# Optimization experiments

Measured on AMD Instinct MI355X. Metric: run time of the kernel, lower is better.

The kernel has to match this reference:

```python
import jax, jax.numpy as jnp
import numpy as np

B, S, D, H = 2, 2048, 1024, 16
HD = D // H
SCALE = HD ** -0.5

def setup_inputs() -> dict:
    key = jax.random.key(0)
    ks = jax.random.split(key, 5)
    x = jax.random.normal(ks[0], (B, S, D), dtype=jnp.float32)
    Wqkv = jax.random.normal(ks[1], (D, 3 * D), dtype=jnp.float32) * (D ** -0.5)
    bqkv = jnp.zeros((3 * D,), dtype=jnp.float32)
    Wproj = jax.random.normal(ks[2], (D, D), dtype=jnp.float32) * (D ** -0.5)
    bproj = jnp.zeros((D,), dtype=jnp.float32)
    return {"x": x, "Wqkv": Wqkv, "bqkv": bqkv, "Wproj": Wproj, "bproj": bproj}

def reference(x, Wqkv, bqkv, Wproj, bproj):
    b, s, _ = x.shape
    qkv = x @ Wqkv + bqkv                       # [B,S,3D]
    qkv = qkv.reshape(b, s, 3, H, HD)
    q, k, v = [jnp.transpose(qkv[:, :, i], (0, 2, 1, 3)) for i in range(3)]  # [B,H,S,HD]
    attn = jnp.einsum('bhqd,bhkd->bhqk', q, k) * SCALE   # [B,H,S,S]
    attn = jax.nn.softmax(attn, axis=-1)
    out = jnp.einsum('bhqk,bhkd->bhqd', attn, v)         # [B,H,S,HD]
    out = jnp.transpose(out, (0, 2, 1, 3)).reshape(b, s, D)
    return out @ Wproj + bproj
```

## Files before the change

kernel.cpp:

```cpp
#include <hip/hip_runtime.h>
#include <hip/hip_bf16.h>

#define BB 2
#define SS 2048
#define DD 1024
#define HH 16
#define HDD 64
#define MM (BB*SS)
#define NQKV (3*DD)
#define SCALE 0.125f
#define QPRESCALE 0.18033688f

typedef __bf16 bf16_t;
typedef bf16_t bf16x4 __attribute__((ext_vector_type(4)));
typedef bf16_t bf16x8 __attribute__((ext_vector_type(8)));
typedef float f32x4 __attribute__((ext_vector_type(4)));
typedef float f32x16 __attribute__((ext_vector_type(16)));

__device__ __forceinline__ void gl_lds16(const bf16_t* g, bf16_t* l) {
    __builtin_amdgcn_global_load_lds(
        (const __attribute__((address_space(1))) unsigned int*)(uintptr_t)g,
        (__attribute__((address_space(3))) unsigned int*)(uintptr_t)l,
        16, 0, 0);
}

__global__ __launch_bounds__(256) void prep(
    const float* __restrict__ x, const float* __restrict__ Wqkv,
    const float* __restrict__ Wproj, bf16_t* __restrict__ xb,
    bf16_t* __restrict__ wqkvt, bf16_t* __restrict__ wprojt)
{
    const int bx = blockIdx.x;
    if (bx < 2048) {
        int i = (bx * 256 + threadIdx.x) * 8;
        float4 a = *(const float4*)(x + i);
        float4 b = *(const float4*)(x + i + 4);
        bf16x8 v;
        v[0]=(bf16_t)a.x; v[1]=(bf16_t)a.y; v[2]=(bf16_t)a.z; v[3]=(bf16_t)a.w;
        v[4]=(bf16_t)b.x; v[5]=(bf16_t)b.y; v[6]=(bf16_t)b.z; v[7]=(bf16_t)b.w;
        *reinterpret_cast<bf16x8*>(xb + i) = v;
        return;
    }
    __shared__ float tile[32][33];
    const float* src; bf16_t* dst; int C, bxl, byl;
    if (bx < 5120) {
        int t = bx - 2048;
        byl = t / 96; bxl = t - byl * 96;
        src = Wqkv;  dst = wqkvt;  C = NQKV;
    } else {
        int t = bx - 5120;
        byl = t >> 5; bxl = t & 31;
        src = Wproj; dst = wprojt; C = DD;
    }
    const int R = DD;
    const int tx = threadIdx.x & 31, ty = threadIdx.x >> 5;
    const int r0 = byl * 32, c0 = bxl * 32;
    #pragma unroll
    for (int i = 0; i < 32; i += 8)
        tile[ty + i][tx] = src[(size_t)(r0 + ty + i) * C + c0 + tx];
    __syncthreads();
    #pragma unroll
    for (int i = 0; i < 32; i += 8)
        dst[(size_t)(c0 + ty + i) * R + r0 + tx] = (bf16_t)tile[tx][ty + i];
}

template <int MODE>
__global__ __launch_bounds__(256) void gemm_bt(
    const bf16_t* __restrict__ A, const bf16_t* __restrict__ Bt,
    const float* __restrict__ bias, float* __restrict__ outf,
    bf16_t* __restrict__ qw, bf16_t* __restrict__ kw, bf16_t* __restrict__ vtw,
    int N, int K)
{
    __shared__ __align__(16) bf16_t As[2][128 * 32];
    __shared__ __align__(16) bf16_t Bs[2][128 * 32];

    const int tid  = threadIdx.x;
    const int w    = tid >> 6;
    const int lane = tid & 63;
    const int lr   = lane & 15;
    const int quad = lane >> 4;
    const int m0   = blockIdx.y * 128;
    const int n0   = blockIdx.x * 128;
    const int wm   = w >> 1;
    const int wn   = w & 1;

    f32x4 acc[4][4];
    #pragma unroll
    for (int i = 0; i < 4; i++)
        #pragma unroll
        for (int j = 0; j < 4; j++) acc[i][j] = (f32x4){0.f, 0.f, 0.f, 0.f};

    const int stgRow = lane >> 2;
    const int stgCol = (lane & 3) * 8;
    const bf16_t* aPtr = A  + (size_t)(m0 + w * 32 + stgRow) * K + stgCol;
    const bf16_t* bPtr = Bt + (size_t)(n0 + w * 32 + stgRow) * K + stgCol;
    const size_t rowSkip = (size_t)16 * K;

    for (int ks = 0; ks < K; ks += 64) {
        __syncthreads();
        #pragma unroll
        for (int s = 0; s < 2; s++) {
            const int ko = ks + s * 32;
            gl_lds16(aPtr + ko,           &As[s][w * 1024]);
            gl_lds16(aPtr + rowSkip + ko, &As[s][w * 1024 + 512]);
            gl_lds16(bPtr + ko,           &Bs[s][w * 1024]);
            gl_lds16(bPtr + rowSkip + ko, &Bs[s][w * 1024 + 512]);
        }
        __syncthreads();

        #pragma unroll
        for (int s = 0; s < 2; s++) {
            bf16x8 af[4], bf[4];
            #pragma unroll
            for (int mi = 0; mi < 4; mi++)
                af[mi] = *reinterpret_cast<const bf16x8*>(&As[s][(wm * 64 + mi * 16 + lr) * 32 + quad * 8]);
            #pragma unroll
            for (int ni = 0; ni < 4; ni++)
                bf[ni] = *reinterpret_cast<const bf16x8*>(&Bs[s][(wn * 64 + ni * 16 + lr) * 32 + quad * 8]);
            #pragma unroll
            for (int mi = 0; mi < 4; mi++)
                #pragma unroll
                for (int ni = 0; ni < 4; ni++)
                    acc[mi][ni] = __builtin_amdgcn_mfma_f32_16x16x32_bf16(af[mi], bf[ni], acc[mi][ni], 0, 0, 0);
        }
    }

    if constexpr (MODE == 0) {
        const int which = n0 >> 10;
        if (which == 2) {
            #pragma unroll
            for (int mi = 0; mi < 4; mi++) {
                #pragma unroll
                for (int ni = 0; ni < 4; ni++) {
                    const int row0 = m0 + wm * 64 + mi * 16 + quad * 4;
                    const int col  = n0 + wn * 64 + ni * 16 + lr;
                    const int b = row0 >> 11, s0 = row0 & 2047;
                    const int d = col & 1023;
                    const int h = d >> 6, hd = d & 63;
                    const float bc = bias[col];
                    bf16x4 v;
                    v[0] = (bf16_t)(acc[mi][ni][0] + bc);
                    v[1] = (bf16_t)(acc[mi][ni][1] + bc);
                    v[2] = (bf16_t)(acc[mi][ni][2] + bc);
                    v[3] = (bf16_t)(acc[mi][ni][3] + bc);
                    *reinterpret_cast<bf16x4*>(
                        &vtw[((size_t)(b * HH + h) * HDD + hd) * SS + s0]) = v;
                }
            }
        } else {
            bf16_t* dst = (which == 0) ? qw : kw;
            const float mul = (which == 0) ? QPRESCALE : 1.f;
            #pragma unroll
            for (int mi = 0; mi < 4; mi++)
                #pragma unroll
                for (int ni = 0; ni < 4; ni++) {
                    const int col = n0 + wn * 64 + ni * 16 + lr;
                    const int d = col & 1023;
                    const int h = d >> 6, hd = d & 63;
                    const float bc = bias[col];
                    #pragma unroll
                    for (int reg = 0; reg < 4; reg++) {
                        const int row = m0 + wm * 64 + mi * 16 + quad * 4 + reg;
                        const int b = row >> 11, s = row & 2047;
                        dst[((size_t)(b * HH + h) * SS + s) * HDD + hd] =
                            (bf16_t)((acc[mi][ni][reg] + bc) * mul);
                    }
                }
        }
    } else {
        #pragma unroll
        for (int mi = 0; mi < 4; mi++)
            #pragma unroll
            for (int ni = 0; ni < 4; ni++)
                #pragma unroll
                for (int reg = 0; reg < 4; reg++) {
                    const int row = m0 + wm * 64 + mi * 16 + quad * 4 + reg;
                    const int col = n0 + wn * 64 + ni * 16 + lr;
                    outf[(size_t)row * N + col] = acc[mi][ni][reg] + bias[col];
                }
    }
}

__global__ __launch_bounds__(256) void gemm_bt64(
    const bf16_t* __restrict__ A, const bf16_t* __restrict__ Bt,
    const float* __restrict__ bias, float* __restrict__ outf, int N, int K)
{
    __shared__ __align__(16) bf16_t As[2][64 * 32];
    __shared__ __align__(16) bf16_t Bs[2][128 * 32];

    const int tid  = threadIdx.x;
    const int w    = tid >> 6;
    const int lane = tid & 63;
    const int lr   = lane & 15;
    const int quad = lane >> 4;
    const int m0   = blockIdx.y * 64;
    const int n0   = blockIdx.x * 128;
    const int wm   = w >> 1;
    const int wn   = w & 1;

    f32x4 acc[2][4];
    #pragma unroll
    for (int i = 0; i < 2; i++)
        #pragma unroll
        for (int j = 0; j < 4; j++) acc[i][j] = (f32x4){0.f, 0.f, 0.f, 0.f};

    const int stgRow = lane >> 2;
    const int stgCol = (lane & 3) * 8;
    const bf16_t* aPtr = A  + (size_t)(m0 + w * 16 + stgRow) * K + stgCol;
    const bf16_t* bPtr = Bt + (size_t)(n0 + w * 32 + stgRow) * K + stgCol;
    const size_t rowSkip = (size_t)16 * K;

    for (int ks = 0; ks < K; ks += 64) {
        __syncthreads();
        #pragma unroll
        for (int s = 0; s < 2; s++) {
            const int ko = ks + s * 32;
            gl_lds16(aPtr + ko,           &As[s][w * 512]);
            gl_lds16(bPtr + ko,           &Bs[s][w * 1024]);
            gl_lds16(bPtr + rowSkip + ko, &Bs[s][w * 1024 + 512]);
        }
        __syncthreads();

        #pragma unroll
        for (int s = 0; s < 2; s++) {
            bf16x8 af[2], bf[4];
            #pragma unroll
            for (int mi = 0; mi < 2; mi++)
                af[mi] = *reinterpret_cast<const bf16x8*>(&As[s][(wm * 32 + mi * 16 + lr) * 32 + quad * 8]);
            #pragma unroll
            for (int ni = 0; ni < 4; ni++)
                bf[ni] = *reinterpret_cast<const bf16x8*>(&Bs[s][(wn * 64 + ni * 16 + lr) * 32 + quad * 8]);
            #pragma unroll
            for (int mi = 0; mi < 2; mi++)
                #pragma unroll
                for (int ni = 0; ni < 4; ni++)
                    acc[mi][ni] = __builtin_amdgcn_mfma_f32_16x16x32_bf16(af[mi], bf[ni], acc[mi][ni], 0, 0, 0);
        }
    }

    #pragma unroll
    for (int mi = 0; mi < 2; mi++)
        #pragma unroll
        for (int ni = 0; ni < 4; ni++)
            #pragma unroll
            for (int reg = 0; reg < 4; reg++) {
                int row = m0 + wm * 32 + mi * 16 + quad * 4 + reg;
                int col = n0 + wn * 64 + ni * 16 + lr;
                outf[(size_t)row * N + col] = acc[mi][ni][reg] + bias[col];
            }
}

__global__ __launch_bounds__(512, 4) void attn_kernel(
    const bf16_t* __restrict__ qws, const bf16_t* __restrict__ kws,
    const bf16_t* __restrict__ vtws, bf16_t* __restrict__ ob)
{
    __shared__ __align__(16) bf16_t smem[17024];
    bf16_t* Ks = smem;
    bf16_t* Vs = smem + 8320;

    const int tid  = threadIdx.x;
    const int w    = tid >> 6;
    const int g    = w >> 2;
    const int wg   = w & 3;
    const int lane = tid & 63;
    const int ln31 = lane & 31;
    const int ln5  = lane >> 5;

    const int qb = blockIdx.x;
    const int bh = blockIdx.y;
    const int b  = bh >> 4;
    const int h  = bh & 15;

    const bf16_t* Qh  = qws  + (size_t)bh * SS * HDD;
    const bf16_t* Kh  = kws  + (size_t)bh * SS * HDD;
    const bf16_t* Vth = vtws + (size_t)bh * HDD * SS;

    const int q0w    = qb * 128 + wg * 32;
    const int kvbase = g * 1024;
    const int kofs   = g * 520;
    const int vofs   = g * 4352;

    bf16x8 aq[4];
    #pragma unroll
    for (int f = 0; f < 4; f++)
        aq[f] = *(const bf16x8*)(Qh + (size_t)(q0w + ln31) * HDD + f * 16 + ln5 * 8);

    const int gtid = tid & 255;
    const int sc = gtid & 7;
    const int sr = gtid >> 3;

    {
        bf16x8 k0 = *(const bf16x8*)(Kh  + (size_t)(kvbase + sr     ) * HDD + sc * 8);
        bf16x8 k1 = *(const bf16x8*)(Kh  + (size_t)(kvbase + sr + 32) * HDD + sc * 8);
        bf16x8 v0 = *(const bf16x8*)(Vth + (size_t)(sr     ) * SS + kvbase + sc * 8);
        bf16x8 v1 = *(const bf16x8*)(Vth + (size_t)(sr + 32) * SS + kvbase + sc * 8);
        *reinterpret_cast<bf16x8*>(&Ks[(kofs + sc * 65 + sr     ) * 8]) = k0;
        *reinterpret_cast<bf16x8*>(&Ks[(kofs + sc * 65 + sr + 32) * 8]) = k1;
        bf16_t* vd0 = &Vs[vofs + (sr     ) * 68 + sc * 8];
        bf16_t* vd1 = &Vs[vofs + (sr + 32) * 68 + sc * 8];
        *reinterpret_cast<bf16x4*>(vd0)     = __builtin_shufflevector(v0, v0, 0,1,2,3);
        *reinterpret_cast<bf16x4*>(vd0 + 4) = __builtin_shufflevector(v0, v0, 4,5,6,7);
        *reinterpret_cast<bf16x4*>(vd1)     = __builtin_shufflevector(v1, v1, 0,1,2,3);
        *reinterpret_cast<bf16x4*>(vd1 + 4) = __builtin_shufflevector(v1, v1, 4,5,6,7);
    }
    __syncthreads();

    float l = 0.f;
    f32x16 o[2];
    #pragma unroll
    for (int nh = 0; nh < 2; nh++)
        #pragma unroll
        for (int r = 0; r < 16; r++) o[nh][r] = 0.f;

    for (int it = 0; it < 16; ++it) {
        f32x16 sfr[2];
        #pragma unroll
        for (int ni = 0; ni < 2; ni++) {
            #pragma unroll
            for (int r = 0; r < 16; r++) sfr[ni][r] = 0.f;
            #pragma unroll
            for (int f = 0; f < 4; f++) {
                bf16x8 kb = *reinterpret_cast<const bf16x8*>(
                    &Ks[(kofs + (2 * f + ln5) * 65 + ni * 32 + ln31) * 8]);
                sfr[ni] = __builtin_amdgcn_mfma_f32_32x32x16_bf16(kb, aq[f], sfr[ni], 0, 0, 0);
            }
        }

        bf16x8 nk0, nk1, nv0, nv1;
        const bool more = (it + 1 < 16);
        if (more) {
            const int kvn = kvbase + (it + 1) * 64;
            nk0 = *(const bf16x8*)(Kh  + (size_t)(kvn + sr     ) * HDD + sc * 8);
            nk1 = *(const bf16x8*)(Kh  + (size_t)(kvn + sr + 32) * HDD + sc * 8);
            nv0 = *(const bf16x8*)(Vth + (size_t)(sr     ) * SS + kvn + sc * 8);
            nv1 = *(const bf16x8*)(Vth + (size_t)(sr + 32) * SS + kvn + sc * 8);
        }

        float p[2][16];
        #pragma unroll
        for (int ni = 0; ni < 2; ni++)
            #pragma unroll
            for (int r = 0; r < 16; r++) {
                p[ni][r] = __builtin_amdgcn_exp2f(sfr[ni][r]);
                l += p[ni][r];
            }

        bf16x8 ap[4];
        #pragma unroll
        for (int c16 = 0; c16 < 4; c16++)
            #pragma unroll
            for (int j = 0; j < 8; j++)
                ap[c16][j] = (bf16_t)p[c16 >> 1][(c16 & 1) * 8 + j];

        #pragma unroll
        for (int nh = 0; nh < 2; nh++) {
            const bf16_t* vrow = &Vs[vofs + (nh * 32 + ln31) * 68];
            #pragma unroll
            for (int c16 = 0; c16 < 4; c16++) {
                bf16x4 lo = *(const bf16x4*)(vrow + c16 * 16 + 4 * ln5);
                bf16x4 hi = *(const bf16x4*)(vrow + c16 * 16 + 8 + 4 * ln5);
                bf16x8 vb = __builtin_shufflevector(lo, hi, 0, 1, 2, 3, 4, 5, 6, 7);
                o[nh] = __builtin_amdgcn_mfma_f32_32x32x16_bf16(ap[c16], vb, o[nh], 0, 0, 0);
            }
        }

        if (more) {
            __syncthreads();
            *reinterpret_cast<bf16x8*>(&Ks[(kofs + sc * 65 + sr     ) * 8]) = nk0;
            *reinterpret_cast<bf16x8*>(&Ks[(kofs + sc * 65 + sr + 32) * 8]) = nk1;
            bf16_t* vd0 = &Vs[vofs + (sr     ) * 68 + sc * 8];
            bf16_t* vd1 = &Vs[vofs + (sr + 32) * 68 + sc * 8];
            *reinterpret_cast<bf16x4*>(vd0)     = __builtin_shufflevector(nv0, nv0, 0,1,2,3);
            *reinterpret_cast<bf16x4*>(vd0 + 4) = __builtin_shufflevector(nv0, nv0, 4,5,6,7);
            *reinterpret_cast<bf16x4*>(vd1)     = __builtin_shufflevector(nv1, nv1, 0,1,2,3);
            *reinterpret_cast<bf16x4*>(vd1 + 4) = __builtin_shufflevector(nv1, nv1, 4,5,6,7);
            __syncthreads();
        }
    }

    l += __shfl_xor(l, 32, 64);

    __syncthreads();
    float* Of = (float*)smem;
    float* Lf = (float*)(smem + 16384);
    if (ln5 == 0) Lf[g * 128 + wg * 32 + ln31] = l;
    if (g == 1) {
        #pragma unroll
        for (int nh = 0; nh < 2; nh++)
            #pragma unroll
            for (int r = 0; r < 16; r++) {
                const int q = (r & 3) + 8 * (r >> 2) + 4 * ln5;
                Of[(wg * 32 + q) * 64 + nh * 32 + ln31] = o[nh][r];
            }
    }
    __syncthreads();
    if (g == 0) {
        float inv[16];
        #pragma unroll
        for (int r = 0; r < 16; r++) {
            const int q = (r & 3) + 8 * (r >> 2) + 4 * ln5;
            inv[r] = 1.f / (Lf[wg * 32 + q] + Lf[128 + wg * 32 + q]);
        }
        #pragma unroll
        for (int nh = 0; nh < 2; nh++)
            #pragma unroll
            for (int r = 0; r < 16; r++) {
                const int q  = (r & 3) + 8 * (r >> 2) + 4 * ln5;
                const int hd = nh * 32 + ln31;
                float val = (o[nh][r] + Of[(wg * 32 + q) * 64 + hd]) * inv[r];
                ob[((size_t)b * SS + q0w + q) * DD + h * HDD + hd] = (bf16_t)val;
            }
    }
}

extern "C" void kernel_launch(void* const* d_in, const int* in_sizes, int n_in,
                              void* d_out, int out_size, void* d_ws, size_t ws_size,
                              hipStream_t stream) {
    const float* x     = (const float*)d_in[0];
    const float* Wqkv  = (const float*)d_in[1];
    const float* bqkv  = (const float*)d_in[2];
    const float* Wproj = (const float*)d_in[3];
    const float* bproj = (const float*)d_in[4];
    float* out = (float*)d_out;

    const size_t NEL = (size_t)MM * DD;
    bf16_t* qws    = (bf16_t*)d_ws;
    bf16_t* kws    = qws  + NEL;
    bf16_t* vtws   = kws  + NEL;
    bf16_t* xb     = vtws + NEL;
    bf16_t* ows    = xb;
    bf16_t* wqkvt  = xb + NEL;
    bf16_t* wprojt = wqkvt + (size_t)NQKV * DD;

    prep<<<6144, 256, 0, stream>>>(x, Wqkv, Wproj, xb, wqkvt, wprojt);

    gemm_bt<0><<<dim3(NQKV / 128, MM / 128), 256, 0, stream>>>(
        xb, wqkvt, bqkv, nullptr, qws, kws, vtws, NQKV, DD);

    attn_kernel<<<dim3(SS / 128, BB * HH), 512, 0, stream>>>(qws, kws, vtws, ows);

    gemm_bt64<<<dim3(DD / 128, MM / 64), 256, 0, stream>>>(
        ows, wprojt, bproj, out, DD, DD);
}
```

Baseline: 191.0 us.

## Split attention KV range across four wave groups; single-stage GEMM K loop

The attention kernel now launches 1024 threads per block. Four wave groups each process a quarter of the key/value sequence, and their partial outputs and row sums are combined through shared memory in a two-step reduction. This shortens each wave's serial KV loop and adds more waves to hide latency, at the cost of larger LDS use, extra barriers, and reduction traffic. Separately, the QKV GEMM drops its two-slice 64-wide K step for a 32-wide step. That halves LDS staging but doubles the number of barrier pairs per tile.

```diff
diff --git a/kernel.cpp b/kernel.cpp
--- a/kernel.cpp
+++ b/kernel.cpp
@@ -70,8 +70,8 @@
     bf16_t* __restrict__ qw, bf16_t* __restrict__ kw, bf16_t* __restrict__ vtw,
     int N, int K)
 {
-    __shared__ __align__(16) bf16_t As[2][128 * 32];
-    __shared__ __align__(16) bf16_t Bs[2][128 * 32];
+    __shared__ __align__(16) bf16_t As[128 * 32];
+    __shared__ __align__(16) bf16_t Bs[128 * 32];
 
     const int tid  = threadIdx.x;
     const int w    = tid >> 6;
@@ -93,35 +93,30 @@
     const int stgCol = (lane & 3) * 8;
     const bf16_t* aPtr = A  + (size_t)(m0 + w * 32 + stgRow) * K + stgCol;
     const bf16_t* bPtr = Bt + (size_t)(n0 + w * 32 + stgRow) * K + stgCol;
+    bf16_t* aDst = As + w * 1024;
+    bf16_t* bDst = Bs + w * 1024;
     const size_t rowSkip = (size_t)16 * K;
 
-    for (int ks = 0; ks < K; ks += 64) {
+    for (int ks = 0; ks < K; ks += 32) {
         __syncthreads();
-        #pragma unroll
-        for (int s = 0; s < 2; s++) {
-            const int ko = ks + s * 32;
-            gl_lds16(aPtr + ko,           &As[s][w * 1024]);
-            gl_lds16(aPtr + rowSkip + ko, &As[s][w * 1024 + 512]);
-            gl_lds16(bPtr + ko,           &Bs[s][w * 1024]);
-            gl_lds16(bPtr + rowSkip + ko, &Bs[s][w * 1024 + 512]);
-        }
+        gl_lds16(aPtr + ks,           aDst);
+        gl_lds16(aPtr + rowSkip + ks, aDst + 512);
+        gl_lds16(bPtr + ks,           bDst);
+        gl_lds16(bPtr + rowSkip + ks, bDst + 512);
         __syncthreads();
 
-        #pragma unroll
-        for (int s = 0; s < 2; s++) {
-            bf16x8 af[4], bf[4];
-            #pragma unroll
-            for (int mi = 0; mi < 4; mi++)
-                af[mi] = *reinterpret_cast<const bf16x8*>(&As[s][(wm * 64 + mi * 16 + lr) * 32 + quad * 8]);
+        bf16x8 af[4], bf[4];
+        #pragma unroll
+        for (int mi = 0; mi < 4; mi++)
+            af[mi] = *reinterpret_cast<const bf16x8*>(&As[(wm * 64 + mi * 16 + lr) * 32 + quad * 8]);
+        #pragma unroll
+        for (int ni = 0; ni < 4; ni++)
+            bf[ni] = *reinterpret_cast<const bf16x8*>(&Bs[(wn * 64 + ni * 16 + lr) * 32 + quad * 8]);
+        #pragma unroll
+        for (int mi = 0; mi < 4; mi++)
             #pragma unroll
             for (int ni = 0; ni < 4; ni++)
-                bf[ni] = *reinterpret_cast<const bf16x8*>(&Bs[s][(wn * 64 + ni * 16 + lr) * 32 + quad * 8]);
-            #pragma unroll
-            for (int mi = 0; mi < 4; mi++)
-                #pragma unroll
-                for (int ni = 0; ni < 4; ni++)
-                    acc[mi][ni] = __builtin_amdgcn_mfma_f32_16x16x32_bf16(af[mi], bf[ni], acc[mi][ni], 0, 0, 0);
-        }
+                acc[mi][ni] = __builtin_amdgcn_mfma_f32_16x16x32_bf16(af[mi], bf[ni], acc[mi][ni], 0, 0, 0);
     }
 
     if constexpr (MODE == 0) {
@@ -249,13 +244,13 @@
             }
 }
 
-__global__ __launch_bounds__(512, 4) void attn_kernel(
+__global__ __launch_bounds__(1024, 8) void attn_kernel(
     const bf16_t* __restrict__ qws, const bf16_t* __restrict__ kws,
     const bf16_t* __restrict__ vtws, bf16_t* __restrict__ ob)
 {
-    __shared__ __align__(16) bf16_t smem[17024];
+    __shared__ __align__(16) bf16_t smem[34048];
     bf16_t* Ks = smem;
-    bf16_t* Vs = smem + 8320;
+    bf16_t* Vs = smem + 16640;
 
     const int tid  = threadIdx.x;
     const int w    = tid >> 6;
@@ -275,7 +270,7 @@
     const bf16_t* Vth = vtws + (size_t)bh * HDD * SS;
 
     const int q0w    = qb * 128 + wg * 32;
-    const int kvbase = g * 1024;
+    const int kvbase = g * 512;
     const int kofs   = g * 520;
     const int vofs   = g * 4352;
 
@@ -311,7 +306,7 @@
         #pragma unroll
         for (int r = 0; r < 16; r++) o[nh][r] = 0.f;
 
-    for (int it = 0; it < 16; ++it) {
+    for (int it = 0; it < 8; ++it) {
         f32x16 sfr[2];
         #pragma unroll
         for (int ni = 0; ni < 2; ni++) {
@@ -326,7 +321,7 @@
         }
 
         bf16x8 nk0, nk1, nv0, nv1;
-        const bool more = (it + 1 < 16);
+        const bool more = (it + 1 < 8);
         if (more) {
             const int kvn = kvbase + (it + 1) * 64;
             nk0 = *(const bf16x8*)(Kh  + (size_t)(kvn + sr     ) * HDD + sc * 8);
@@ -380,10 +375,12 @@
     l += __shfl_xor(l, 32, 64);
 
     __syncthreads();
-    float* Of = (float*)smem;
-    float* Lf = (float*)(smem + 16384);
+    float* Of0 = (float*)smem;
+    float* Of1 = (float*)(smem + 16384);
+    float* Lf  = (float*)(smem + 32768);
     if (ln5 == 0) Lf[g * 128 + wg * 32 + ln31] = l;
-    if (g == 1) {
+    if (g == 1 || g == 3) {
+        float* Of = (g == 1) ? Of0 : Of1;
         #pragma unroll
         for (int nh = 0; nh < 2; nh++)
             #pragma unroll
@@ -393,12 +390,34 @@
             }
     }
     __syncthreads();
+    if (g == 0 || g == 2) {
+        const float* Of = (g == 0) ? Of0 : Of1;
+        #pragma unroll
+        for (int nh = 0; nh < 2; nh++)
+            #pragma unroll
+            for (int r = 0; r < 16; r++) {
+                const int q = (r & 3) + 8 * (r >> 2) + 4 * ln5;
+                o[nh][r] += Of[(wg * 32 + q) * 64 + nh * 32 + ln31];
+            }
+    }
+    __syncthreads();
+    if (g == 2) {
+        #pragma unroll
+        for (int nh = 0; nh < 2; nh++)
+            #pragma unroll
+            for (int r = 0; r < 16; r++) {
+                const int q = (r & 3) + 8 * (r >> 2) + 4 * ln5;
+                Of0[(wg * 32 + q) * 64 + nh * 32 + ln31] = o[nh][r];
+            }
+    }
+    __syncthreads();
     if (g == 0) {
         float inv[16];
         #pragma unroll
         for (int r = 0; r < 16; r++) {
             const int q = (r & 3) + 8 * (r >> 2) + 4 * ln5;
-            inv[r] = 1.f / (Lf[wg * 32 + q] + Lf[128 + wg * 32 + q]);
+            const int qi = wg * 32 + q;
+            inv[r] = 1.f / (Lf[qi] + Lf[128 + qi] + Lf[256 + qi] + Lf[384 + qi]);
         }
         #pragma unroll
         for (int nh = 0; nh < 2; nh++)
@@ -406,7 +425,7 @@
             for (int r = 0; r < 16; r++) {
                 const int q  = (r & 3) + 8 * (r >> 2) + 4 * ln5;
                 const int hd = nh * 32 + ln31;
-                float val = (o[nh][r] + Of[(wg * 32 + q) * 64 + hd]) * inv[r];
+                float val = (o[nh][r] + Of0[(wg * 32 + q) * 64 + hd]) * inv[r];
                 ob[((size_t)b * SS + q0w + q) * DD + h * HDD + hd] = (bf16_t)val;
             }
     }
@@ -436,7 +455,7 @@
     gemm_bt<0><<<dim3(NQKV / 128, MM / 128), 256, 0, stream>>>(
         xb, wqkvt, bqkv, nullptr, qws, kws, vtws, NQKV, DD);
 
-    attn_kernel<<<dim3(SS / 128, BB * HH), 512, 0, stream>>>(qws, kws, vtws, ows);
+    attn_kernel<<<dim3(SS / 128, BB * HH), 1024, 0, stream>>>(qws, kws, vtws, ows);
 
     gemm_bt64<<<dim3(DD / 128, MM / 64), 256, 0, stream>>>(
         ows, wprojt, bproj, out, DD, DD);
```

Result: slower. 712.8 us (+273.2%).

## Double-buffer K/V tiles in attention and shrink GEMM K-step to 32

Applied to the files above, without the earlier changes.

The attention kernel now ping-pongs between two shared-memory K/V buffers. Each iteration writes the next tile into the other buffer and needs one barrier instead of two. The GEMM drops from two 32-wide LDS stages per barrier pair to one, halving its LDS footprint but doubling the number of synchronisation rounds. Attention shared memory doubles to about 68KB per 512-thread block, which may reduce how many blocks fit on a CU.

```diff
diff --git a/kernel.cpp b/kernel.cpp
--- a/kernel.cpp
+++ b/kernel.cpp
@@ -70,8 +70,8 @@
     bf16_t* __restrict__ qw, bf16_t* __restrict__ kw, bf16_t* __restrict__ vtw,
     int N, int K)
 {
-    __shared__ __align__(16) bf16_t As[2][128 * 32];
-    __shared__ __align__(16) bf16_t Bs[2][128 * 32];
+    __shared__ __align__(16) bf16_t As[128 * 32];
+    __shared__ __align__(16) bf16_t Bs[128 * 32];
 
     const int tid  = threadIdx.x;
     const int w    = tid >> 6;
@@ -93,35 +93,30 @@
     const int stgCol = (lane & 3) * 8;
     const bf16_t* aPtr = A  + (size_t)(m0 + w * 32 + stgRow) * K + stgCol;
     const bf16_t* bPtr = Bt + (size_t)(n0 + w * 32 + stgRow) * K + stgCol;
+    bf16_t* aDst = As + w * 1024;
+    bf16_t* bDst = Bs + w * 1024;
     const size_t rowSkip = (size_t)16 * K;
 
-    for (int ks = 0; ks < K; ks += 64) {
+    for (int ks = 0; ks < K; ks += 32) {
         __syncthreads();
-        #pragma unroll
-        for (int s = 0; s < 2; s++) {
-            const int ko = ks + s * 32;
-            gl_lds16(aPtr + ko,           &As[s][w * 1024]);
-            gl_lds16(aPtr + rowSkip + ko, &As[s][w * 1024 + 512]);
-            gl_lds16(bPtr + ko,           &Bs[s][w * 1024]);
-            gl_lds16(bPtr + rowSkip + ko, &Bs[s][w * 1024 + 512]);
-        }
+        gl_lds16(aPtr + ks,           aDst);
+        gl_lds16(aPtr + rowSkip + ks, aDst + 512);
+        gl_lds16(bPtr + ks,           bDst);
+        gl_lds16(bPtr + rowSkip + ks, bDst + 512);
         __syncthreads();
 
-        #pragma unroll
-        for (int s = 0; s < 2; s++) {
-            bf16x8 af[4], bf[4];
-            #pragma unroll
-            for (int mi = 0; mi < 4; mi++)
-                af[mi] = *reinterpret_cast<const bf16x8*>(&As[s][(wm * 64 + mi * 16 + lr) * 32 + quad * 8]);
+        bf16x8 af[4], bf[4];
+        #pragma unroll
+        for (int mi = 0; mi < 4; mi++)
+            af[mi] = *reinterpret_cast<const bf16x8*>(&As[(wm * 64 + mi * 16 + lr) * 32 + quad * 8]);
+        #pragma unroll
+        for (int ni = 0; ni < 4; ni++)
+            bf[ni] = *reinterpret_cast<const bf16x8*>(&Bs[(wn * 64 + ni * 16 + lr) * 32 + quad * 8]);
+        #pragma unroll
+        for (int mi = 0; mi < 4; mi++)
             #pragma unroll
             for (int ni = 0; ni < 4; ni++)
-                bf[ni] = *reinterpret_cast<const bf16x8*>(&Bs[s][(wn * 64 + ni * 16 + lr) * 32 + quad * 8]);
-            #pragma unroll
-            for (int mi = 0; mi < 4; mi++)
-                #pragma unroll
-                for (int ni = 0; ni < 4; ni++)
-                    acc[mi][ni] = __builtin_amdgcn_mfma_f32_16x16x32_bf16(af[mi], bf[ni], acc[mi][ni], 0, 0, 0);
-        }
+                acc[mi][ni] = __builtin_amdgcn_mfma_f32_16x16x32_bf16(af[mi], bf[ni], acc[mi][ni], 0, 0, 0);
     }
 
     if constexpr (MODE == 0) {
@@ -253,9 +248,9 @@
     const bf16_t* __restrict__ qws, const bf16_t* __restrict__ kws,
     const bf16_t* __restrict__ vtws, bf16_t* __restrict__ ob)
 {
-    __shared__ __align__(16) bf16_t smem[17024];
+    __shared__ __align__(16) bf16_t smem[34048];
     bf16_t* Ks = smem;
-    bf16_t* Vs = smem + 8320;
+    bf16_t* Vs = smem + 16640;
 
     const int tid  = threadIdx.x;
     const int w    = tid >> 6;
@@ -276,8 +271,6 @@
 
     const int q0w    = qb * 128 + wg * 32;
     const int kvbase = g * 1024;
-    const int kofs   = g * 520;
-    const int vofs   = g * 4352;
 
     bf16x8 aq[4];
     #pragma unroll
@@ -289,14 +282,16 @@
     const int sr = gtid >> 3;
 
     {
+        const int ko = g * 520;
+        const int vo = g * 4352;
         bf16x8 k0 = *(const bf16x8*)(Kh  + (size_t)(kvbase + sr     ) * HDD + sc * 8);
         bf16x8 k1 = *(const bf16x8*)(Kh  + (size_t)(kvbase + sr + 32) * HDD + sc * 8);
         bf16x8 v0 = *(const bf16x8*)(Vth + (size_t)(sr     ) * SS + kvbase + sc * 8);
         bf16x8 v1 = *(const bf16x8*)(Vth + (size_t)(sr + 32) * SS + kvbase + sc * 8);
-        *reinterpret_cast<bf16x8*>(&Ks[(kofs + sc * 65 + sr     ) * 8]) = k0;
-        *reinterpret_cast<bf16x8*>(&Ks[(kofs + sc * 65 + sr + 32) * 8]) = k1;
-        bf16_t* vd0 = &Vs[vofs + (sr     ) * 68 + sc * 8];
-        bf16_t* vd1 = &Vs[vofs + (sr + 32) * 68 + sc * 8];
+        *reinterpret_cast<bf16x8*>(&Ks[(ko + sc * 65 + sr     ) * 8]) = k0;
+        *reinterpret_cast<bf16x8*>(&Ks[(ko + sc * 65 + sr + 32) * 8]) = k1;
+        bf16_t* vd0 = &Vs[vo + (sr     ) * 68 + sc * 8];
+        bf16_t* vd1 = &Vs[vo + (sr + 32) * 68 + sc * 8];
         *reinterpret_cast<bf16x4*>(vd0)     = __builtin_shufflevector(v0, v0, 0,1,2,3);
         *reinterpret_cast<bf16x4*>(vd0 + 4) = __builtin_shufflevector(v0, v0, 4,5,6,7);
         *reinterpret_cast<bf16x4*>(vd1)     = __builtin_shufflevector(v1, v1, 0,1,2,3);
@@ -311,7 +306,11 @@
         #pragma unroll
         for (int r = 0; r < 16; r++) o[nh][r] = 0.f;
 
+    int buf = 0;
     for (int it = 0; it < 16; ++it) {
+        const int ko = buf * 1040 + g * 520;
+        const int vo = buf * 8704 + g * 4352;
+
         f32x16 sfr[2];
         #pragma unroll
         for (int ni = 0; ni < 2; ni++) {
@@ -320,7 +319,7 @@
             #pragma unroll
             for (int f = 0; f < 4; f++) {
                 bf16x8 kb = *reinterpret_cast<const bf16x8*>(
-                    &Ks[(kofs + (2 * f + ln5) * 65 + ni * 32 + ln31) * 8]);
+                    &Ks[(ko + (2 * f + ln5) * 65 + ni * 32 + ln31) * 8]);
                 sfr[ni] = __builtin_amdgcn_mfma_f32_32x32x16_bf16(kb, aq[f], sfr[ni], 0, 0, 0);
             }
         }
@@ -353,7 +352,7 @@
 
         #pragma unroll
         for (int nh = 0; nh < 2; nh++) {
-            const bf16_t* vrow = &Vs[vofs + (nh * 32 + ln31) * 68];
+            const bf16_t* vrow = &Vs[vo + (nh * 32 + ln31) * 68];
             #pragma unroll
             for (int c16 = 0; c16 < 4; c16++) {
                 bf16x4 lo = *(const bf16x4*)(vrow + c16 * 16 + 4 * ln5);
@@ -364,17 +363,19 @@
         }
 
         if (more) {
-            __syncthreads();
-            *reinterpret_cast<bf16x8*>(&Ks[(kofs + sc * 65 + sr     ) * 8]) = nk0;
-            *reinterpret_cast<bf16x8*>(&Ks[(kofs + sc * 65 + sr + 32) * 8]) = nk1;
-            bf16_t* vd0 = &Vs[vofs + (sr     ) * 68 + sc * 8];
-            bf16_t* vd1 = &Vs[vofs + (sr + 32) * 68 + sc * 8];
+            const int ko1 = (buf ^ 1) * 1040 + g * 520;
+            const int vo1 = (buf ^ 1) * 8704 + g * 4352;
+            *reinterpret_cast<bf16x8*>(&Ks[(ko1 + sc * 65 + sr     ) * 8]) = nk0;
+            *reinterpret_cast<bf16x8*>(&Ks[(ko1 + sc * 65 + sr + 32) * 8]) = nk1;
+            bf16_t* vd0 = &Vs[vo1 + (sr     ) * 68 + sc * 8];
+            bf16_t* vd1 = &Vs[vo1 + (sr + 32) * 68 + sc * 8];
             *reinterpret_cast<bf16x4*>(vd0)     = __builtin_shufflevector(nv0, nv0, 0,1,2,3);
             *reinterpret_cast<bf16x4*>(vd0 + 4) = __builtin_shufflevector(nv0, nv0, 4,5,6,7);
             *reinterpret_cast<bf16x4*>(vd1)     = __builtin_shufflevector(nv1, nv1, 0,1,2,3);
             *reinterpret_cast<bf16x4*>(vd1 + 4) = __builtin_shufflevector(nv1, nv1, 4,5,6,7);
-            __syncthreads();
-        }
+        }
+        __syncthreads();
+        buf ^= 1;
     }
 
     l += __shfl_xor(l, 32, 64);
```

Result: slower. 197.7 us (+3.5%).
